# Performance work log

Hardware: AMD Instinct MI355X
Metric: run time of the kernel (lower is better)

The kernel has to match this reference:

```python
import jax, jax.numpy as jnp
import numpy as np

B, N, T, D, O = 8, 1024, 12, 64, 64

def setup_inputs() -> dict:
    key = jax.random.key(0)
    k1, k2, k3 = jax.random.split(key, 3)
    x = jax.random.normal(k1, (B, N, T, D), dtype=jnp.float32)
    # row-normalized random adjacency (dense mask, as in the torch module)
    adj = jax.random.uniform(k2, (N, N), dtype=jnp.float32)
    norm_adj = adj / jnp.sum(adj, axis=-1, keepdims=True)
    theta_w = jax.random.normal(k3, (D, O), dtype=jnp.float32) / np.sqrt(D)
    return {"x": x, "norm_adj": norm_adj, "theta_w": theta_w}

def reference(x, norm_adj, theta_w):
    b, n, t, d = x.shape
    # [B, N, T, D] -> [B*T, N, D]
    xr = jnp.transpose(x, (0, 2, 1, 3)).reshape(b * t, n, d)
    # spatial attention scores [B*T, N, N]
    scores = jnp.einsum('gnd,gmd->gnm', xr, xr) / jnp.sqrt(jnp.float32(d))
    attn = jax.nn.softmax(scores, axis=-1)
    # adjacency-masked attention, then aggregate and project
    agg = jnp.einsum('gnm,gmd->gnd', norm_adj[None, :, :] * attn, xr)
    out = jnp.einsum('gnd,do->gno', agg, theta_w)
    # [B*T, N, O] -> [B, N, T, O], relu
    out = jnp.transpose(out.reshape(b, t, n, -1), (0, 2, 1, 3))
    return jax.nn.relu(out)
```

## Files before the change

### kernel.cpp

```cpp
#include <hip/hip_runtime.h>


#define NB    8
#define NT    12
#define NNODE 1024
#define ND    64
#define XROW  768
#define NG    96

typedef __bf16 bf16x8 __attribute__((ext_vector_type(8)));
typedef __bf16 bf16x4 __attribute__((ext_vector_type(4)));
typedef float  floatx4 __attribute__((ext_vector_type(4)));

#define MFMA(a,b,c) __builtin_amdgcn_mfma_f32_16x16x32_bf16((a),(b),(c),0,0,0)

#define QSCALE 0.18033688011112042f

#define OKH 0
#define OKL 4096
#define OWH 8192
#define OWL 12288
#define BUF2 16384
#define SMEM12 (2 * BUF2)
#define KSTRIDE 72
#define VSTRIDE 40
#define PSTRIDE 36
#define AGSTRIDE 68
#define OFF_KHI 0
#define OFF_KLO 4608
#define OFF_VHI 9216
#define OFF_VLO 14336
#define OFF_P   19456
#define SMEM_FB (19456 + 128*PSTRIDE*4)

#define WXHI  0
#define WXLO  6291456
#define WVPHI 12582912
#define WVPLO 18874368
#define WS_BYTES 50348032ULL

struct bfpair { __bf16 h, l; };

__device__ __forceinline__ bfpair split1(float f) {
    bfpair r;
    __bf16 hb = (__bf16)f;
    float hf = __builtin_bit_cast(float,
                   (unsigned)__builtin_bit_cast(unsigned short, hb) << 16);
    r.h = hb;
    r.l = (__bf16)(f - hf);
    return r;
}

__device__ __forceinline__ void gld16(const __bf16* g, char* l) {
    __builtin_amdgcn_global_load_lds(
        (const __attribute__((address_space(1))) void*)g,
        (__attribute__((address_space(3))) void*)l, 16, 0, 0);
}

__global__ void __launch_bounds__(256)
presplit(const float* __restrict__ x, const float* __restrict__ theta,
         __bf16* __restrict__ ws)
{
    __shared__ __align__(16) float T[64 * 68];
    __shared__ __align__(16) float Wt[64 * 68];
    const int tid  = threadIdx.x;
    const int lane = tid & 63;
    const int wave = tid >> 6;
    const int l16  = lane & 15;
    const int quad = lane >> 4;
    const int bx   = blockIdx.x;
    const int g    = bx >> 4;
    const int nblk = bx & 15;
    const int bb   = g / NT;
    const int tt   = g - bb * NT;
    const int n0   = nblk * 64;

    __bf16* Xhi  = ws + WXHI  + (size_t)g * 65536;
    __bf16* Xlo  = ws + WXLO  + (size_t)g * 65536;
    __bf16* WPhi = ws + WVPHI + (size_t)g * 65536;
    __bf16* WPlo = ws + WVPLO + (size_t)g * 65536;
    const float* xg = x + (size_t)bb * (NNODE * XROW) + (size_t)tt * ND;

    #pragma unroll
    for (int i = 0; i < 4; ++i) {
        int chunk = i * 256 + tid;
        int n  = chunk >> 4;
        int c4 = (chunk & 15) * 4;
        floatx4 f = *(const floatx4*)(xg + (size_t)(n0 + n) * XROW + c4);
        *(floatx4*)(T + n * 68 + c4) = f;
        bf16x4 h, l;
        #pragma unroll
        for (int j = 0; j < 4; ++j) {
            bfpair p = split1(f[j]); h[j] = p.h; l[j] = p.l;
        }
        *(bf16x4*)(Xhi + (size_t)(n0 + n) * 64 + c4) = h;
        *(bf16x4*)(Xlo + (size_t)(n0 + n) * 64 + c4) = l;
    }
    __syncthreads();

    {
        bf16x8 tah[2], tal[2];
        #pragma unroll
        for (int ks = 0; ks < 2; ++ks)
            #pragma unroll
            for (int j = 0; j < 8; ++j) {
                bfpair p = split1(T[(wave*16 + l16)*68 + ks*32 + quad*8 + j]);
                tah[ks][j] = p.h; tal[ks][j] = p.l;
            }
        const floatx4 vz = {0.f, 0.f, 0.f, 0.f};
        #pragma unroll
        for (int ot = 0; ot < 4; ++ot) {
            bf16x8 thb[2], tlb[2];
            #pragma unroll
            for (int ks = 0; ks < 2; ++ks)
                #pragma unroll
                for (int j = 0; j < 8; ++j) {
                    bfpair p = split1(theta[(size_t)(ks*32 + quad*8 + j) * ND
                                            + ot*16 + l16]);
                    thb[ks][j] = p.h; tlb[ks][j] = p.l;
                }
            floatx4 Wc = vz;
            #pragma unroll
            for (int ks = 0; ks < 2; ++ks) {
                Wc = MFMA(tah[ks], thb[ks], Wc);
                Wc = MFMA(tal[ks], thb[ks], Wc);
                Wc = MFMA(tah[ks], tlb[ks], Wc);
            }
            #pragma unroll
            for (int r = 0; r < 4; ++r)
                Wt[(wave*16 + quad*4 + r)*68 + ot*16 + l16] = Wc[r];
        }
    }
    __syncthreads();

    {
        const int o  = tid >> 2;
        const int nc = (tid & 3) * 16;
        const int tb = nc & 32;
        bf16x8 h0, l0, h1, l1;
        #pragma unroll
        for (int j = 0; j < 8; ++j) {
            int c0 = (nc & 31) + j;
            int k0 = ((c0 & 7) >> 2) * 16 + (c0 >> 3) * 4 + (c0 & 3);
            bfpair p = split1(Wt[(tb + k0) * 68 + o]);
            h0[j] = p.h; l0[j] = p.l;
            int c1 = (nc & 31) + 8 + j;
            int k1 = ((c1 & 7) >> 2) * 16 + (c1 >> 3) * 4 + (c1 & 3);
            bfpair q = split1(Wt[(tb + k1) * 68 + o]);
            h1[j] = q.h; l1[j] = q.l;
        }
        __bf16* dsth = WPhi + (size_t)o * NNODE + n0 + nc;
        __bf16* dstl = WPlo + (size_t)o * NNODE + n0 + nc;
        *(bf16x8*)dsth = h0; *(bf16x8*)(dsth + 8) = h1;
        *(bf16x8*)dstl = l0; *(bf16x8*)(dstl + 8) = l1;
    }
}

__global__ void __launch_bounds__(256, 3)
spattn12(const __bf16* __restrict__ ws, const float* __restrict__ adj,
         float* __restrict__ out)
{
    __shared__ __align__(16) char smem[SMEM12];

    const int tid  = threadIdx.x;
    const int wave = tid >> 6;
    const int lane = tid & 63;
    const int l16  = lane & 15;
    const int quad = lane >> 4;

    const int bx   = blockIdx.x;
    const int g    = bx % NG;
    const int rblk = bx / NG;
    const int bb   = g / NT;
    const int tt   = g - bb * NT;
    const int row0 = rblk * 128;

    const __bf16* xh  = ws + WXHI  + (size_t)g * 65536;
    const __bf16* xl  = ws + WXLO  + (size_t)g * 65536;
    const __bf16* wph = ws + WVPHI + (size_t)g * 65536;
    const __bf16* wpl = ws + WVPLO + (size_t)g * 65536;

    const int kc   = (lane & 7) ^ (lane >> 3);
    const int krow = (wave << 3) + (lane >> 3);
    const int wo   = ((wave << 3) + (lane >> 3)) * 2 + ((kc & 4) >> 2);
    const int wko  = (kc & 3) * 8;

    bf16x8 qhi[2][2], qlo[2][2];
    #pragma unroll
    for (int mt = 0; mt < 2; ++mt) {
        const __bf16* q0 = xh + (size_t)(row0 + wave*32 + mt*16 + l16) * 64 + quad*8;
        const __bf16* q1 = xl + (size_t)(row0 + wave*32 + mt*16 + l16) * 64 + quad*8;
        #pragma unroll
        for (int ks = 0; ks < 2; ++ks) {
            qhi[mt][ks] = *(const bf16x8*)(q0 + ks*32);
            qlo[mt][ks] = *(const bf16x8*)(q1 + ks*32);
        }
    }

    const floatx4 vzero = {0.f, 0.f, 0.f, 0.f};
    floatx4 acc[2][4];
    #pragma unroll
    for (int mt = 0; mt < 2; ++mt)
        #pragma unroll
        for (int dt = 0; dt < 4; ++dt)
            acc[mt][dt] = vzero;
    float lpart[2] = {0.f, 0.f};

    {
        char* b0 = smem;
        gld16(xh  + (size_t)krow * 64 + kc*8,          b0 + OKH + wave*1024);
        gld16(xl  + (size_t)krow * 64 + kc*8,          b0 + OKL + wave*1024);
        gld16(wph + (size_t)wo * NNODE + wko,          b0 + OWH + wave*1024);
        gld16(wpl + (size_t)wo * NNODE + wko,          b0 + OWL + wave*1024);
    }

    int cur = 0;
    for (int ct = 0; ct < 32; ++ct) {
        const int key0 = ct * 32;
        __syncthreads();
        if (ct < 31) {
            const int nk = key0 + 32;
            char* wb = smem + (cur ^ 1) * BUF2;
            gld16(xh  + (size_t)(nk + krow) * 64 + kc*8, wb + OKH + wave*1024);
            gld16(xl  + (size_t)(nk + krow) * 64 + kc*8, wb + OKL + wave*1024);
            gld16(wph + (size_t)wo * NNODE + nk + wko,   wb + OWH + wave*1024);
            gld16(wpl + (size_t)wo * NNODE + nk + wko,   wb + OWL + wave*1024);
        }
        floatx4 av[2][2];
        #pragma unroll
        for (int mt = 0; mt < 2; ++mt)
            #pragma unroll
            for (int nt = 0; nt < 2; ++nt)
                av[mt][nt] = *(const floatx4*)(adj
                    + (size_t)(row0 + wave*32 + mt*16 + l16) * NNODE
                    + key0 + nt*16 + quad*4);

        char* rb = smem + cur * BUF2;
        __bf16* Khi = (__bf16*)(rb + OKH);
        __bf16* Klo = (__bf16*)(rb + OKL);
        __bf16* Whi = (__bf16*)(rb + OWH);
        __bf16* Wlo = (__bf16*)(rb + OWL);

        floatx4 S[2][2] = {{vzero, vzero}, {vzero, vzero}};
        __builtin_amdgcn_s_setprio(1);
        #pragma unroll
        for (int ks = 0; ks < 2; ++ks) {
            #pragma unroll
            for (int nt = 0; nt < 2; ++nt) {
                const int kch = (((ks*4 + quad) ^ (l16 & 7))) * 8;
                bf16x8 ah = *(const bf16x8*)(Khi + (nt*16 + l16)*64 + kch);
                bf16x8 al = *(const bf16x8*)(Klo + (nt*16 + l16)*64 + kch);
                #pragma unroll
                for (int mt = 0; mt < 2; ++mt) {
                    S[mt][nt] = MFMA(ah, qhi[mt][ks], S[mt][nt]);
                    S[mt][nt] = MFMA(ah, qlo[mt][ks], S[mt][nt]);
                    S[mt][nt] = MFMA(al, qhi[mt][ks], S[mt][nt]);
                }
            }
        }
        __builtin_amdgcn_s_setprio(0);

        bf16x8 pah[2], pal[2];
        #pragma unroll
        for (int mt = 0; mt < 2; ++mt)
            #pragma unroll
            for (int nt = 0; nt < 2; ++nt)
                #pragma unroll
                for (int r = 0; r < 4; ++r) {
                    float w = __builtin_amdgcn_exp2f(S[mt][nt][r] * QSCALE);
                    lpart[mt] += w;
                    bfpair pp = split1(av[mt][nt][r] * w);
                    pah[mt][nt*4 + r] = pp.h;
                    pal[mt][nt*4 + r] = pp.l;
                }

        __builtin_amdgcn_s_setprio(1);
        #pragma unroll
        for (int dt = 0; dt < 4; ++dt) {
            const int wmr = dt*8 + (l16 >> 1);
            const int wch = ((((l16 & 1)*4 + quad) ^ ((l16 >> 1) & 7))) * 8;
            bf16x8 wvh = *(const bf16x8*)(Whi + wmr*64 + wch);
            bf16x8 wvl = *(const bf16x8*)(Wlo + wmr*64 + wch);
            #pragma unroll
            for (int mt = 0; mt < 2; ++mt) {
                acc[mt][dt] = MFMA(pah[mt], wvh, acc[mt][dt]);
                acc[mt][dt] = MFMA(pal[mt], wvh, acc[mt][dt]);
                acc[mt][dt] = MFMA(pah[mt], wvl, acc[mt][dt]);
            }
        }
        __builtin_amdgcn_s_setprio(0);
        cur ^= 1;
    }

    float linv[2][4];
    #pragma unroll
    for (int mt = 0; mt < 2; ++mt) {
        float lv = lpart[mt];
        lv += __shfl_xor(lv, 16);
        lv += __shfl_xor(lv, 32);
        #pragma unroll
        for (int r = 0; r < 4; ++r)
            linv[mt][r] = 1.0f / __shfl(lv, quad*4 + r);
    }

    float* obase = out + (size_t)bb * (NNODE * XROW) + tt * ND;
    #pragma unroll
    for (int mt = 0; mt < 2; ++mt)
        #pragma unroll
        for (int dt = 0; dt < 4; ++dt)
            #pragma unroll
            for (int r = 0; r < 4; ++r) {
                float v = acc[mt][dt][r] * linv[mt][r];
                obase[(size_t)(row0 + wave*32 + mt*16 + quad*4 + r) * XROW + dt*16 + l16]
                    = v > 0.f ? v : 0.f;
            }
}

__global__ void __launch_bounds__(256, 2)
spattn_fb(const float* __restrict__ x, const float* __restrict__ adj,
          const float* __restrict__ theta, float* __restrict__ out)
{
    __shared__ __align__(16) char smem[SMEM_FB];
    __bf16* Khi = (__bf16*)(smem + OFF_KHI);
    __bf16* Klo = (__bf16*)(smem + OFF_KLO);
    __bf16* Vhi = (__bf16*)(smem + OFF_VHI);
    __bf16* Vlo = (__bf16*)(smem + OFF_VLO);
    float*  Pm  = (float*)(smem + OFF_P);

    const int tid  = threadIdx.x;
    const int wave = tid >> 6;
    const int lane = tid & 63;
    const int l16  = lane & 15;
    const int quad = lane >> 4;

    const int bx   = blockIdx.x;
    const int g    = bx >> 3;
    const int rblk = bx & 7;
    const int bb   = g / NT;
    const int tt   = g - bb * NT;
    const int row0 = rblk * 128;

    const float* xbase = x + (size_t)bb * (NNODE * XROW) + tt * ND;

    bf16x8 qhi[2][2], qlo[2][2];
    #pragma unroll
    for (int mt = 0; mt < 2; ++mt) {
        const float* qsrc = xbase + (size_t)(row0 + wave*32 + mt*16 + l16) * XROW;
        #pragma unroll
        for (int ks = 0; ks < 2; ++ks) {
            floatx4 f0 = *(const floatx4*)(qsrc + ks*32 + quad*8);
            floatx4 f1 = *(const floatx4*)(qsrc + ks*32 + quad*8 + 4);
            #pragma unroll
            for (int i = 0; i < 4; ++i) {
                bfpair p0 = split1(f0[i]*QSCALE);
                qhi[mt][ks][i]   = p0.h; qlo[mt][ks][i]   = p0.l;
                bfpair p1 = split1(f1[i]*QSCALE);
                qhi[mt][ks][4+i] = p1.h; qlo[mt][ks][4+i] = p1.l;
            }
        }
    }

    const floatx4 vzero = {0.f, 0.f, 0.f, 0.f};
    floatx4 acc[2][4];
    #pragma unroll
    for (int mt = 0; mt < 2; ++mt)
        #pragma unroll
        for (int dt = 0; dt < 4; ++dt)
            acc[mt][dt] = vzero;
    float lpart[2][4] = {{0.f,0.f,0.f,0.f},{0.f,0.f,0.f,0.f}};

    const int skey = tid >> 3;
    const int sd0  = (tid & 7) * 8;
    const int svd  = tid >> 2;
    const int svk0 = (tid & 3) * 8;
    floatx4 kf0, kf1;
    float vf[8];

    {
        const float* ksrc = xbase + (size_t)skey * XROW + sd0;
        kf0 = *(const floatx4*)ksrc;
        kf1 = *(const floatx4*)(ksrc + 4);
        const float* vsrc = xbase + (size_t)svk0 * XROW + svd;
        #pragma unroll
        for (int i = 0; i < 8; ++i) vf[i] = vsrc[i * XROW];
    }

    for (int ct = 0; ct < 32; ++ct) {
        const int key0 = ct * 32;
        __syncthreads();
        {
            bf16x8 h, l;
            #pragma unroll
            for (int i = 0; i < 4; ++i) {
                bfpair p0 = split1(kf0[i]); h[i]   = p0.h; l[i]   = p0.l;
                bfpair p1 = split1(kf1[i]); h[4+i] = p1.h; l[4+i] = p1.l;
            }
            *(bf16x8*)(Khi + skey*KSTRIDE + sd0) = h;
            *(bf16x8*)(Klo + skey*KSTRIDE + sd0) = l;
            bf16x8 vh, vl;
            #pragma unroll
            for (int i = 0; i < 8; ++i) {
                bfpair p = split1(vf[i]); vh[i] = p.h; vl[i] = p.l;
            }
            *(bf16x8*)(Vhi + svd*VSTRIDE + svk0) = vh;
            *(bf16x8*)(Vlo + svd*VSTRIDE + svk0) = vl;
        }
        __syncthreads();
        if (ct < 31) {
            const int nk = key0 + 32;
            const float* ksrc = xbase + (size_t)(nk + skey) * XROW + sd0;
            kf0 = *(const floatx4*)ksrc;
            kf1 = *(const floatx4*)(ksrc + 4);
            const float* vsrc = xbase + (size_t)(nk + svk0) * XROW + svd;
            #pragma unroll
            for (int i = 0; i < 8; ++i) vf[i] = vsrc[i * XROW];
        }
        float av[2][2][4];
        #pragma unroll
        for (int mt = 0; mt < 2; ++mt)
            #pragma unroll
            for (int nt = 0; nt < 2; ++nt)
                #pragma unroll
                for (int r = 0; r < 4; ++r)
                    av[mt][nt][r] = adj[(size_t)(row0 + wave*32 + mt*16 + quad*4 + r) * NNODE
                                        + key0 + nt*16 + l16];

        floatx4 S[2][2] = {{vzero, vzero}, {vzero, vzero}};
        #pragma unroll
        for (int ks = 0; ks < 2; ++ks) {
            #pragma unroll
            for (int nt = 0; nt < 2; ++nt) {
                bf16x8 bh = *(const bf16x8*)(Khi + (nt*16 + l16)*KSTRIDE + ks*32 + quad*8);
                bf16x8 bl = *(const bf16x8*)(Klo + (nt*16 + l16)*KSTRIDE + ks*32 + quad*8);
                #pragma unroll
                for (int mt = 0; mt < 2; ++mt) {
                    S[mt][nt] = MFMA(qhi[mt][ks], bh, S[mt][nt]);
                    S[mt][nt] = MFMA(qlo[mt][ks], bh, S[mt][nt]);
                    S[mt][nt] = MFMA(qhi[mt][ks], bl, S[mt][nt]);
                }
            }
        }
        #pragma unroll
        for (int mt = 0; mt < 2; ++mt)
            #pragma unroll
            for (int nt = 0; nt < 2; ++nt)
                #pragma unroll
                for (int r = 0; r < 4; ++r) {
                    float w = __builtin_amdgcn_exp2f(S[mt][nt][r]);
                    lpart[mt][r] += w;
                    Pm[(wave*32 + mt*16 + quad*4 + r)*PSTRIDE + nt*16 + l16] = av[mt][nt][r] * w;
                }
        bf16x8 pah[2], pal[2];
        #pragma unroll
        for (int mt = 0; mt < 2; ++mt) {
            const float* pp = Pm + (wave*32 + mt*16 + l16)*PSTRIDE + quad*8;
            floatx4 p0 = *(const floatx4*)pp;
            floatx4 p1 = *(const floatx4*)(pp + 4);
            #pragma unroll
            for (int i = 0; i < 4; ++i) {
                bfpair q0 = split1(p0[i]); pah[mt][i]   = q0.h; pal[mt][i]   = q0.l;
                bfpair q1 = split1(p1[i]); pah[mt][4+i] = q1.h; pal[mt][4+i] = q1.l;
            }
        }
        #pragma unroll
        for (int dt = 0; dt < 4; ++dt) {
            bf16x8 vh = *(const bf16x8*)(Vhi + (dt*16 + l16)*VSTRIDE + quad*8);
            bf16x8 vl = *(const bf16x8*)(Vlo + (dt*16 + l16)*VSTRIDE + quad*8);
            #pragma unroll
            for (int mt = 0; mt < 2; ++mt) {
                acc[mt][dt] = MFMA(pah[mt], vh, acc[mt][dt]);
                acc[mt][dt] = MFMA(pal[mt], vh, acc[mt][dt]);
                acc[mt][dt] = MFMA(pah[mt], vl, acc[mt][dt]);
            }
        }
    }

    float linv[2][4];
    #pragma unroll
    for (int mt = 0; mt < 2; ++mt)
        #pragma unroll
        for (int r = 0; r < 4; ++r) {
            float lv = lpart[mt][r];
            lv += __shfl_xor(lv, 1);
            lv += __shfl_xor(lv, 2);
            lv += __shfl_xor(lv, 4);
            lv += __shfl_xor(lv, 8);
            linv[mt][r] = 1.0f / lv;
        }

    __syncthreads();
    float* AG = (float*)smem;
    #pragma unroll
    for (int mt = 0; mt < 2; ++mt)
        #pragma unroll
        for (int dt = 0; dt < 4; ++dt)
            #pragma unroll
            for (int r = 0; r < 4; ++r)
                AG[(wave*32 + mt*16 + quad*4 + r)*AGSTRIDE + dt*16 + l16]
                    = acc[mt][dt][r] * linv[mt][r];

    bf16x8 th[4][2], tl[4][2];
    #pragma unroll
    for (int ot = 0; ot < 4; ++ot)
        #pragma unroll
        for (int ks = 0; ks < 2; ++ks)
            #pragma unroll
            for (int j = 0; j < 8; ++j) {
                float tv = theta[(ks*32 + quad*8 + j)*ND + ot*16 + l16];
                bfpair p = split1(tv);
                th[ot][ks][j] = p.h; tl[ot][ks][j] = p.l;
            }

    floatx4 oacc[2][4];
    #pragma unroll
    for (int mt = 0; mt < 2; ++mt)
        #pragma unroll
        for (int ot = 0; ot < 4; ++ot)
            oacc[mt][ot] = vzero;
    __syncthreads();
    #pragma unroll
    for (int ks = 0; ks < 2; ++ks) {
        bf16x8 ah[2], al[2];
        #pragma unroll
        for (int mt = 0; mt < 2; ++mt) {
            const float* ap = AG + (wave*32 + mt*16 + l16)*AGSTRIDE + ks*32 + quad*8;
            floatx4 a0 = *(const floatx4*)ap;
            floatx4 a1 = *(const floatx4*)(ap + 4);
            #pragma unroll
            for (int i = 0; i < 4; ++i) {
                bfpair q0 = split1(a0[i]); ah[mt][i]   = q0.h; al[mt][i]   = q0.l;
                bfpair q1 = split1(a1[i]); ah[mt][4+i] = q1.h; al[mt][4+i] = q1.l;
            }
        }
        #pragma unroll
        for (int ot = 0; ot < 4; ++ot)
            #pragma unroll
            for (int mt = 0; mt < 2; ++mt) {
                oacc[mt][ot] = MFMA(ah[mt], th[ot][ks], oacc[mt][ot]);
                oacc[mt][ot] = MFMA(al[mt], th[ot][ks], oacc[mt][ot]);
                oacc[mt][ot] = MFMA(ah[mt], tl[ot][ks], oacc[mt][ot]);
            }
    }

    float* obase = out + (size_t)bb * (NNODE * XROW) + tt * ND;
    #pragma unroll
    for (int mt = 0; mt < 2; ++mt)
        #pragma unroll
        for (int ot = 0; ot < 4; ++ot)
            #pragma unroll
            for (int r = 0; r < 4; ++r) {
                float v = oacc[mt][ot][r];
                obase[(size_t)(row0 + wave*32 + mt*16 + quad*4 + r) * XROW + ot*16 + l16]
                    = v > 0.f ? v : 0.f;
            }
}

extern "C" void kernel_launch(void* const* d_in, const int* in_sizes, int n_in,
                              void* d_out, int out_size, void* d_ws, size_t ws_size,
                              hipStream_t stream) {
    (void)in_sizes; (void)n_in; (void)out_size;
    const float* x     = (const float*)d_in[0];
    const float* adj   = (const float*)d_in[1];
    const float* theta = (const float*)d_in[2];
    float* out = (float*)d_out;
    if (d_ws != nullptr && ws_size >= WS_BYTES) {
        __bf16* ws = (__bf16*)d_ws;
        presplit<<<dim3(1536), dim3(256), 0, stream>>>(x, theta, ws);
        spattn12<<<dim3(768), dim3(256), 0, stream>>>(ws, adj, out);
    } else {
        spattn_fb<<<dim3(768), dim3(256), 0, stream>>>(x, adj, theta, out);
    }
}
```

Measured before the change: 166.4 us.

## Software-pipeline PV MFMAs one tile behind QK with triple-buffered LDS

Restructures the key-tile loop so the P·V' accumulation for tile ct-1 runs after the QK MFMAs of tile ct, overlapping the exp/split VALU work with matrix ops from a different stage. It moves from double to triple buffering of K/W tiles in LDS, rotating three buffer indices, and adds an epilogue for the final tile. Occupancy hint drops from 3 to 2 blocks per CU because LDS grows to 48KB and P fragments stay live across iterations, which increases register pressure.

```diff
diff --git a/kernel.cpp b/kernel.cpp
--- a/kernel.cpp
+++ b/kernel.cpp
@@ -21,7 +21,7 @@
 #define OWH 8192
 #define OWL 12288
 #define BUF2 16384
-#define SMEM12 (2 * BUF2)
+#define SMEM13 (3 * BUF2)
 #define KSTRIDE 72
 #define VSTRIDE 40
 #define PSTRIDE 36
@@ -156,11 +156,11 @@
     }
 }
 
-__global__ void __launch_bounds__(256, 3)
-spattn12(const __bf16* __restrict__ ws, const float* __restrict__ adj,
+__global__ void __launch_bounds__(256, 2)
+spattn13(const __bf16* __restrict__ ws, const float* __restrict__ adj,
          float* __restrict__ out)
 {
-    __shared__ __align__(16) char smem[SMEM12];
+    __shared__ __align__(16) char smem[SMEM13];
 
     const int tid  = threadIdx.x;
     const int wave = tid >> 6;
@@ -205,22 +205,20 @@
         for (int dt = 0; dt < 4; ++dt)
             acc[mt][dt] = vzero;
     float lpart[2] = {0.f, 0.f};
-
-    {
-        char* b0 = smem;
-        gld16(xh  + (size_t)krow * 64 + kc*8,          b0 + OKH + wave*1024);
-        gld16(xl  + (size_t)krow * 64 + kc*8,          b0 + OKL + wave*1024);
-        gld16(wph + (size_t)wo * NNODE + wko,          b0 + OWH + wave*1024);
-        gld16(wpl + (size_t)wo * NNODE + wko,          b0 + OWL + wave*1024);
-    }
-
-    int cur = 0;
+    bf16x8 pah_prev[2], pal_prev[2];
+
+    gld16(xh  + (size_t)krow * 64 + kc*8, smem + OKH + wave*1024);
+    gld16(xl  + (size_t)krow * 64 + kc*8, smem + OKL + wave*1024);
+    gld16(wph + (size_t)wo * NNODE + wko, smem + OWH + wave*1024);
+    gld16(wpl + (size_t)wo * NNODE + wko, smem + OWL + wave*1024);
+
+    int bK = 0, bW = 2, bL = 1;
     for (int ct = 0; ct < 32; ++ct) {
         const int key0 = ct * 32;
         __syncthreads();
         if (ct < 31) {
             const int nk = key0 + 32;
-            char* wb = smem + (cur ^ 1) * BUF2;
+            char* wb = smem + bL * BUF2;
             gld16(xh  + (size_t)(nk + krow) * 64 + kc*8, wb + OKH + wave*1024);
             gld16(xl  + (size_t)(nk + krow) * 64 + kc*8, wb + OKL + wave*1024);
             gld16(wph + (size_t)wo * NNODE + nk + wko,   wb + OWH + wave*1024);
@@ -235,12 +233,9 @@
                     + (size_t)(row0 + wave*32 + mt*16 + l16) * NNODE
                     + key0 + nt*16 + quad*4);
 
-        char* rb = smem + cur * BUF2;
-        __bf16* Khi = (__bf16*)(rb + OKH);
-        __bf16* Klo = (__bf16*)(rb + OKL);
-        __bf16* Whi = (__bf16*)(rb + OWH);
-        __bf16* Wlo = (__bf16*)(rb + OWL);
-
+        char* rbK = smem + bK * BUF2;
+        __bf16* Khi = (__bf16*)(rbK + OKH);
+        __bf16* Klo = (__bf16*)(rbK + OKL);
         floatx4 S[2][2] = {{vzero, vzero}, {vzero, vzero}};
         __builtin_amdgcn_s_setprio(1);
         #pragma unroll
@@ -260,7 +255,27 @@
         }
         __builtin_amdgcn_s_setprio(0);
 
-        bf16x8 pah[2], pal[2];
+        if (ct > 0) {
+            char* rbW = smem + bW * BUF2;
+            __bf16* Whi = (__bf16*)(rbW + OWH);
+            __bf16* Wlo = (__bf16*)(rbW + OWL);
+            __builtin_amdgcn_s_setprio(1);
+            #pragma unroll
+            for (int dt = 0; dt < 4; ++dt) {
+                const int wmr = dt*8 + (l16 >> 1);
+                const int wch = ((((l16 & 1)*4 + quad) ^ ((l16 >> 1) & 7))) * 8;
+                bf16x8 wvh = *(const bf16x8*)(Whi + wmr*64 + wch);
+                bf16x8 wvl = *(const bf16x8*)(Wlo + wmr*64 + wch);
+                #pragma unroll
+                for (int mt = 0; mt < 2; ++mt) {
+                    acc[mt][dt] = MFMA(pah_prev[mt], wvh, acc[mt][dt]);
+                    acc[mt][dt] = MFMA(pal_prev[mt], wvh, acc[mt][dt]);
+                    acc[mt][dt] = MFMA(pah_prev[mt], wvl, acc[mt][dt]);
+                }
+            }
+            __builtin_amdgcn_s_setprio(0);
+        }
+
         #pragma unroll
         for (int mt = 0; mt < 2; ++mt)
             #pragma unroll
@@ -270,11 +285,17 @@
                     float w = __builtin_amdgcn_exp2f(S[mt][nt][r] * QSCALE);
                     lpart[mt] += w;
                     bfpair pp = split1(av[mt][nt][r] * w);
-                    pah[mt][nt*4 + r] = pp.h;
-                    pal[mt][nt*4 + r] = pp.l;
+                    pah_prev[mt][nt*4 + r] = pp.h;
+                    pal_prev[mt][nt*4 + r] = pp.l;
                 }
 
-        __builtin_amdgcn_s_setprio(1);
+        int tmp = bW; bW = bK; bK = bL; bL = tmp;
+    }
+
+    {
+        char* rbW = smem + bW * BUF2;
+        __bf16* Whi = (__bf16*)(rbW + OWH);
+        __bf16* Wlo = (__bf16*)(rbW + OWL);
         #pragma unroll
         for (int dt = 0; dt < 4; ++dt) {
             const int wmr = dt*8 + (l16 >> 1);
@@ -283,13 +304,11 @@
             bf16x8 wvl = *(const bf16x8*)(Wlo + wmr*64 + wch);
             #pragma unroll
             for (int mt = 0; mt < 2; ++mt) {
-                acc[mt][dt] = MFMA(pah[mt], wvh, acc[mt][dt]);
-                acc[mt][dt] = MFMA(pal[mt], wvh, acc[mt][dt]);
-                acc[mt][dt] = MFMA(pah[mt], wvl, acc[mt][dt]);
-            }
-        }
-        __builtin_amdgcn_s_setprio(0);
-        cur ^= 1;
+                acc[mt][dt] = MFMA(pah_prev[mt], wvh, acc[mt][dt]);
+                acc[mt][dt] = MFMA(pal_prev[mt], wvh, acc[mt][dt]);
+                acc[mt][dt] = MFMA(pah_prev[mt], wvl, acc[mt][dt]);
+            }
+        }
     }
 
     float linv[2][4];
@@ -566,7 +585,7 @@
     if (d_ws != nullptr && ws_size >= WS_BYTES) {
         __bf16* ws = (__bf16*)d_ws;
         presplit<<<dim3(1536), dim3(256), 0, stream>>>(x, theta, ws);
-        spattn12<<<dim3(768), dim3(256), 0, stream>>>(ws, adj, out);
+        spattn13<<<dim3(768), dim3(256), 0, stream>>>(ws, adj, out);
     } else {
         spattn_fb<<<dim3(768), dim3(256), 0, stream>>>(x, adj, theta, out);
     }
```

After: 167.2 us. No clear change (+0.5%).
